# Kernel optimization log

Measured on AMD Instinct MI355X. Metric: run time of the kernel, lower is better.

The kernel has to match this reference:

```python
import jax, jax.numpy as jnp
import numpy as np

E = 8          # n_experts
TOPK = 2       # n_activated_experts
ROUTE_SCALE = 1.0
W_SCALE = 0.05  # keep conv outputs in a sane range


def _conv2d_same(x, w):
    # x: (B, Cin, H, W), w: (Cout, Cin, kh, kw) -> (B, Cout, H, W)
    return jax.lax.conv_general_dilated(
        x, w, window_strides=(1, 1), padding='SAME',
        dimension_numbers=('NCHW', 'OIHW', 'NCHW'))


def setup_inputs() -> dict:
    key = jax.random.key(0)
    ks = jax.random.split(key, 6)
    B, Cin, Cout, H, W = 4, 128, 128, 96, 96
    x = jax.random.normal(ks[0], (B, Cin, H, W), dtype=jnp.float32)
    gate_w = jax.random.normal(ks[1], (E, Cin, 3, 3), dtype=jnp.float32) * W_SCALE
    gate_bias = jnp.zeros((E,), dtype=jnp.float32)  # load-balance bias buffer (zeros in eval)
    expert_w = jax.random.normal(ks[2], (E, Cout, Cin, 3, 3), dtype=jnp.float32) * W_SCALE
    expert_b = jax.random.normal(ks[3], (E, Cout), dtype=jnp.float32) * W_SCALE
    shared_w = jax.random.normal(ks[4], (Cout, Cin, 3, 3), dtype=jnp.float32) * W_SCALE
    shared_b = jax.random.normal(ks[5], (Cout,), dtype=jnp.float32) * W_SCALE
    return {'x': x, 'gate_w': gate_w, 'gate_bias': gate_bias,
            'expert_w': expert_w, 'expert_b': expert_b,
            'shared_w': shared_w, 'shared_b': shared_b}


def reference(x, gate_w, gate_bias, expert_w, expert_b, shared_w, shared_b):
    B, Cin, H, W = x.shape
    Cout = shared_w.shape[0]

    # ---- Gate: sigmoid(conv) + bias buffer, per-pixel top-k over expert dim ----
    scores = jax.nn.sigmoid(_conv2d_same(x, gate_w))          # (B, E, H, W)
    biased = scores + gate_bias[None, :, None, None]
    scores_l = jnp.moveaxis(scores, 1, -1)                    # (B, H, W, E)
    biased_l = jnp.moveaxis(biased, 1, -1)
    _, idx = jax.lax.top_k(biased_l, TOPK)                    # (B, H, W, K)
    w_topk = jnp.take_along_axis(scores_l, idx, axis=-1)      # unbiased scores at topk
    w_topk = jax.nn.softmax(w_topk, axis=-1) * ROUTE_SCALE    # (B, H, W, K)

    # Per-pixel per-expert score: scatter topk weights back to E slots.
    onehot = jax.nn.one_hot(idx, E, dtype=x.dtype)            # (B, H, W, K, E)
    score_full = jnp.einsum('bhwke,bhwk->behw', onehot, w_topk)  # (B, E, H, W)

    # ---- Dense expert convs (all experts), then weighted accumulate ----
    ew = expert_w.reshape(E * Cout, Cin, 3, 3)
    eout = _conv2d_same(x, ew).reshape(B, E, Cout, H, W)
    eout = eout + expert_b[None, :, :, None, None]
    output = jnp.einsum('bechw,behw->bchw', eout, score_full)  # (B, Cout, H, W)

    # ---- Shared expert ----
    output = output + _conv2d_same(x, shared_w) + shared_b[None, :, None, None]
    return output
```

## Files before the change

### kernel.cpp

```cpp
#include <hip/hip_runtime.h>
#include <hip/hip_bf16.h>
#include <math.h>


typedef __attribute__((ext_vector_type(8))) short short8;
typedef __attribute__((ext_vector_type(4))) float f32x4;

static __device__ __forceinline__ unsigned short f2bf(float f) {
    unsigned int u = __float_as_uint(f);
    unsigned int r = (u + 0x7FFFu + ((u >> 16) & 1u)) >> 16;
    return (unsigned short)r;
}

__global__ __launch_bounds__(256) void gate_prep_kernel(
    const float* __restrict__ x, const float* __restrict__ gw,
    const float* __restrict__ gb,
    const float* __restrict__ ew, const float* __restrict__ sw,
    float* __restrict__ scores, unsigned short* __restrict__ pw)
{
    __shared__ alignas(16) char smem[45056];
    const int t  = threadIdx.x;
    const int bx = blockIdx.x;

    if (bx >= 576) {
        unsigned short* lt2 = reinterpret_cast<unsigned short*>(smem);
        const int pblk = bx - 576;
        const int e  = pblk >> 4;
        const int wv = (pblk >> 2) & 3;
        const int kc = pblk & 3;
        const float* src = (e < 8) ? (ew + e * 147456) : sw;
        const float* sb2 = src + (wv * 32) * 1152 + kc * 288;

        #pragma unroll
        for (int j = 0; j < 36; ++j) {
            int i = t + j * 256;
            int co_l = i / 288;
            int r    = i - co_l * 288;
            int k_l  = r / 9;
            int tap  = r - k_l * 9;
            float v = sb2[co_l * 1152 + r];
            lt2[tap * 1024 + (co_l >> 4) * 512 +
                ((k_l >> 3) * 16 + (co_l & 15)) * 8 + (k_l & 7)] = f2bf(v);
        }
        __syncthreads();

        uint4* pw16 = reinterpret_cast<uint4*>(pw);
        for (int c = t; c < 1152; c += 256) {
            int tap = c >> 7;
            int rem = c & 127;
            uint4 val = *reinterpret_cast<const uint4*>(&lt2[tap * 1024 + rem * 8]);
            pw16[(e * 9 + tap) * 2048 + wv * 512 + kc * 128 + rem] = val;
        }
        return;
    }

    float* gws = reinterpret_cast<float*>(smem);
    float (*red)[64][8] = reinterpret_cast<float (*)[64][8]>(smem + 36864);

    for (int i = t; i < 9216; i += 256) {
        int ci  = i / 72;
        int r   = i - ci * 72;
        int tap = r >> 3;
        int e   = r & 7;
        gws[i] = gw[(e * 128 + ci) * 9 + tap];
    }
    __syncthreads();

    const int g  = t >> 6;
    const int p  = t & 63;
    const int wt = bx % 3;
    const int h2 = (bx / 3) % 48;
    const int b  = bx / 144;
    const int h  = h2 * 2 + (p >> 5);
    const int w  = wt * 32 + (p & 31);

    int off[9]; float msk[9];
    #pragma unroll
    for (int kh = 0; kh < 3; kh++) {
        #pragma unroll
        for (int kw = 0; kw < 3; kw++) {
            int hh = h + kh - 1, ww = w + kw - 1;
            bool valid = (hh >= 0 && hh < 96 && ww >= 0 && ww < 96);
            int hc = min(max(hh, 0), 95), wc = min(max(ww, 0), 95);
            off[kh * 3 + kw] = hc * 96 + wc;
            msk[kh * 3 + kw] = valid ? 1.0f : 0.0f;
        }
    }

    const float* xb = x + (b * 128 + g * 32) * 9216;
    float acc[8] = {0.f,0.f,0.f,0.f,0.f,0.f,0.f,0.f};
    #pragma unroll 2
    for (int ci = 0; ci < 32; ci++) {
        const float* xc = xb + ci * 9216;
        const f32x4* wr4 = reinterpret_cast<const f32x4*>(&gws[(g * 32 + ci) * 72]);
        float xv[9];
        #pragma unroll
        for (int tap = 0; tap < 9; tap++) xv[tap] = xc[off[tap]] * msk[tap];
        #pragma unroll
        for (int tap = 0; tap < 9; tap++) {
            const f32x4 wa = wr4[tap * 2];
            const f32x4 wb = wr4[tap * 2 + 1];
            #pragma unroll
            for (int e0 = 0; e0 < 4; e0++) {
                acc[e0]     += xv[tap] * wa[e0];
                acc[e0 + 4] += xv[tap] * wb[e0];
            }
        }
    }

    #pragma unroll
    for (int e = 0; e < 8; e++) red[g][p][e] = acc[e];
    __syncthreads();

    if (t < 64) {
        float s[8], bs[8];
        #pragma unroll
        for (int e = 0; e < 8; e++) {
            float v = red[0][t][e] + red[1][t][e] + red[2][t][e] + red[3][t][e];
            s[e]  = 1.0f / (1.0f + expf(-v));
            bs[e] = s[e] + gb[e];
        }
        int i1 = 0; float b1 = bs[0]; float w1 = s[0];
        #pragma unroll
        for (int e = 1; e < 8; e++)
            if (bs[e] > b1) { b1 = bs[e]; i1 = e; w1 = s[e]; }
        int i2 = -1; float b2 = -1e30f; float w2 = 0.f;
        #pragma unroll
        for (int e = 0; e < 8; e++)
            if (e != i1 && bs[e] > b2) { b2 = bs[e]; i2 = e; w2 = s[e]; }

        float mx = fmaxf(w1, w2);
        float e1 = expf(w1 - mx), e2 = expf(w2 - mx);
        float inv = 1.0f / (e1 + e2);
        float p1 = e1 * inv, p2 = e2 * inv;

        const int hh = h2 * 2 + (t >> 5);
        const int ww = wt * 32 + (t & 31);
        int base = b * 8 * 9216 + hh * 96 + ww;
        #pragma unroll
        for (int e = 0; e < 8; e++) {
            float v = (e == i1) ? p1 : ((e == i2) ? p2 : 0.0f);
            scores[base + e * 9216] = v;
        }
    }
}

__global__ __launch_bounds__(256, 3) void moe_main_kernel(
    const float* __restrict__ x, const unsigned short* __restrict__ pw,
    const float* __restrict__ scores, const float* __restrict__ eb,
    const float* __restrict__ sb, float* __restrict__ out)
{
    __shared__ unsigned short xs[4 * 34 * 136];
    __shared__ float sc[8][64];
    __shared__ float bia[9][128];

    const int t  = threadIdx.x;
    const int bx = blockIdx.x;
    const int wt = bx % 3;
    const int h2 = (bx / 3) % 48;
    const int b  = bx / 144;
    const int h0 = h2 * 2, w0 = wt * 32;

    const float* xb = x + b * 128 * 9216;
    for (int i = t; i < 17408; i += 256) {
        int ci  = i / 136;
        int rem = i - ci * 136;
        int row = rem / 34;
        int col = rem - row * 34;
        int hh = h0 - 1 + row;
        int ww = w0 - 1 + col;
        float v = 0.0f;
        if (hh >= 0 && hh < 96 && ww >= 0 && ww < 96)
            v = xb[ci * 9216 + hh * 96 + ww];
        xs[(row * 34 + col) * 136 + ci] = f2bf(v);
    }
    for (int i = t; i < 512; i += 256) {
        int e = i >> 6, p = i & 63;
        sc[e][p] = scores[(b * 8 + e) * 9216 + (h0 + (p >> 5)) * 96 + (w0 + (p & 31))];
    }
    for (int i = t; i < 1152; i += 256) {
        int e = i >> 7, co = i & 127;
        bia[e][co] = (e < 8) ? eb[(e << 7) + co] : sb[co];
    }
    __syncthreads();

    const int wv = t >> 6;
    const int l  = t & 63;
    const int lm = l & 15;
    const int lq = l >> 4;

    f32x4 acc[2][4], accE[2][4];
    #pragma unroll
    for (int i2 = 0; i2 < 2; i2++)
        #pragma unroll
        for (int j = 0; j < 4; j++) {
            acc[i2][j]  = (f32x4){0.f, 0.f, 0.f, 0.f};
            accE[i2][j] = (f32x4){0.f, 0.f, 0.f, 0.f};
        }

    const int bBase = lm * 136 + lq * 8;
    const uint4* pw4 = reinterpret_cast<const uint4*>(pw) + wv * 512 + l;

    uint4 afA[8], afB[8];

#define LOADF(dst, etv) {                                                     \
    const uint4* _p = pw4 + (etv) * 2048;                                     \
    _Pragma("unroll")                                                         \
    for (int q = 0; q < 8; ++q) dst[q] = _p[(q >> 1) * 128 + (q & 1) * 64];   \
}

#define COMPUTE(src, etv) {                                                   \
    const int e_   = (etv) / 9;                                               \
    const int tap_ = (etv) - e_ * 9;                                          \
    const int kh_  = tap_ / 3;                                                \
    const int kw_  = tap_ - kh_ * 3;                                          \
    const int xr0  = kh_ * 4624 + kw_ * 136 + bBase;                          \
    _Pragma("unroll")                                                         \
    for (int kc = 0; kc < 4; ++kc) {                                          \
        const short8 a0 = *reinterpret_cast<const short8*>(&src[kc * 2 + 0]); \
        const short8 a1 = *reinterpret_cast<const short8*>(&src[kc * 2 + 1]); \
        _Pragma("unroll")                                                     \
        for (int j = 0; j < 4; ++j) {                                         \
            const short8 bv = *reinterpret_cast<const short8*>(               \
                &xs[xr0 + (j >> 1) * 4624 + (j & 1) * 2176 + kc * 32]);       \
            accE[0][j] = __builtin_amdgcn_mfma_f32_16x16x32_bf16(             \
                a0, bv, accE[0][j], 0, 0, 0);                                 \
            accE[1][j] = __builtin_amdgcn_mfma_f32_16x16x32_bf16(             \
                a1, bv, accE[1][j], 0, 0, 0);                                 \
        }                                                                     \
    }                                                                         \
    if (tap_ == 8) {                  \
        _Pragma("unroll")                                                     \
        for (int j = 0; j < 4; ++j) {                                         \
            const int p = j * 16 + lm;                                        \
            const float s_ = (e_ < 8) ? sc[e_][p] : 1.0f;                     \
            _Pragma("unroll")                                                 \
            for (int i2 = 0; i2 < 2; ++i2)                                    \
                _Pragma("unroll")                                             \
                for (int rr = 0; rr < 4; ++rr) {                              \
                    const int co_ = wv * 32 + i2 * 16 + lq * 4 + rr;          \
                    acc[i2][j][rr] += s_ * (accE[i2][j][rr] + bia[e_][co_]);  \
                    accE[i2][j][rr] = 0.f;                                    \
                }                                                             \
        }                                                                     \
    }                                                                         \
}

    LOADF(afA, 0);
    for (int eu = 0; eu < 40; ++eu) {
        const int et0 = eu * 2;
        LOADF(afB, et0 + 1);
        COMPUTE(afA, et0);
        LOADF(afA, et0 + 2);
        COMPUTE(afB, et0 + 1);
    }
    COMPUTE(afA, 80);
#undef COMPUTE
#undef LOADF

    float* ob = out + b * 128 * 9216;
    #pragma unroll
    for (int i2 = 0; i2 < 2; i2++)
        #pragma unroll
        for (int rr = 0; rr < 4; rr++) {
            const int co = wv * 32 + i2 * 16 + lq * 4 + rr;
            #pragma unroll
            for (int j = 0; j < 4; j++) {
                const int hh = h0 + (j >> 1);
                const int ww = w0 + (j & 1) * 16 + lm;
                ob[co * 9216 + hh * 96 + ww] = acc[i2][j][rr];
            }
        }
}

extern "C" void kernel_launch(void* const* d_in, const int* in_sizes, int n_in,
                              void* d_out, int out_size, void* d_ws, size_t ws_size,
                              hipStream_t stream) {
    const float* x  = (const float*)d_in[0];
    const float* gw = (const float*)d_in[1];
    const float* gb = (const float*)d_in[2];
    const float* ew = (const float*)d_in[3];
    const float* eb = (const float*)d_in[4];
    const float* sw = (const float*)d_in[5];
    const float* sb = (const float*)d_in[6];
    float* out = (float*)d_out;

    unsigned short* pw = (unsigned short*)d_ws;
    float* scores = (float*)((char*)d_ws + 2654208);

    gate_prep_kernel<<<720, 256, 0, stream>>>(x, gw, gb, ew, sw, scores, pw);
    moe_main_kernel<<<576, 256, 0, stream>>>(x, pw, scores, eb, sb, out);
}
```

Baseline: 221.1 us.

## Pad LDS pixel stride to 132 and keep gate weights in registers via readlane

The main kernel's x tile in shared memory now uses a per-pixel stride of 132 instead of 136 bf16, and the B operand is read as two 8-byte halves. The intent is to cut LDS bank conflicts on the MFMA operand reads. In the gate kernel, the staging of gate weights through shared memory is removed. Each lane now holds 36 weights in registers that are broadcast with readlane inside a fully unrolled channel loop, which avoids the LDS fill, its barrier and repeated LDS reads. The cost is higher register pressure and many scalar readlane instructions, and the 8-byte-aligned loads may issue more LDS instructions.

New measurement: 234.2 us. +5.9%, slower.

```diff
diff --git a/kernel.cpp b/kernel.cpp
--- a/kernel.cpp
+++ b/kernel.cpp
@@ -4,12 +4,23 @@
 
 
 typedef __attribute__((ext_vector_type(8))) short short8;
+typedef __attribute__((ext_vector_type(4))) short short4s;
 typedef __attribute__((ext_vector_type(4))) float f32x4;
 
 static __device__ __forceinline__ unsigned short f2bf(float f) {
     unsigned int u = __float_as_uint(f);
     unsigned int r = (u + 0x7FFFu + ((u >> 16) & 1u)) >> 16;
     return (unsigned short)r;
+}
+
+static __device__ __forceinline__ short8 ldsB(const unsigned short* p) {
+    short4s lo = *reinterpret_cast<const short4s*>(p);
+    short4s hi = *reinterpret_cast<const short4s*>(p + 4);
+    return __builtin_shufflevector(lo, hi, 0, 1, 2, 3, 4, 5, 6, 7);
+}
+
+static __device__ __forceinline__ float rdlane(float v, int lane) {
+    return __uint_as_float(__builtin_amdgcn_readlane(__float_as_uint(v), lane));
 }
 
 __global__ __launch_bounds__(256) void gate_prep_kernel(
@@ -18,12 +29,13 @@
     const float* __restrict__ ew, const float* __restrict__ sw,
     float* __restrict__ scores, unsigned short* __restrict__ pw)
 {
-    __shared__ alignas(16) char smem[45056];
+    __shared__ float red[4][64][8];
+    __shared__ unsigned short lt2[9216];
+
     const int t  = threadIdx.x;
     const int bx = blockIdx.x;
 
     if (bx >= 576) {
-        unsigned short* lt2 = reinterpret_cast<unsigned short*>(smem);
         const int pblk = bx - 576;
         const int e  = pblk >> 4;
         const int wv = (pblk >> 2) & 3;
@@ -54,18 +66,6 @@
         return;
     }
 
-    float* gws = reinterpret_cast<float*>(smem);
-    float (*red)[64][8] = reinterpret_cast<float (*)[64][8]>(smem + 36864);
-
-    for (int i = t; i < 9216; i += 256) {
-        int ci  = i / 72;
-        int r   = i - ci * 72;
-        int tap = r >> 3;
-        int e   = r & 7;
-        gws[i] = gw[(e * 128 + ci) * 9 + tap];
-    }
-    __syncthreads();
-
     const int g  = t >> 6;
     const int p  = t & 63;
     const int wt = bx % 3;
@@ -74,6 +74,19 @@
     const int h  = h2 * 2 + (p >> 5);
     const int w  = wt * 32 + (p & 31);
 
+    float wreg[36];
+    {
+        const int ci  = g * 32 + (p >> 1);
+        const int jb  = (p & 1) * 36;
+        #pragma unroll
+        for (int jj = 0; jj < 36; ++jj) {
+            int jglob = jb + jj;
+            int e   = jglob / 9;
+            int tap = jglob - e * 9;
+            wreg[jj] = gw[(e * 128 + ci) * 9 + tap];
+        }
+    }
+
     int off[9]; float msk[9];
     #pragma unroll
     for (int kh = 0; kh < 3; kh++) {
@@ -89,21 +102,20 @@
 
     const float* xb = x + (b * 128 + g * 32) * 9216;
     float acc[8] = {0.f,0.f,0.f,0.f,0.f,0.f,0.f,0.f};
-    #pragma unroll 2
+    #pragma unroll
     for (int ci = 0; ci < 32; ci++) {
         const float* xc = xb + ci * 9216;
-        const f32x4* wr4 = reinterpret_cast<const f32x4*>(&gws[(g * 32 + ci) * 72]);
         float xv[9];
         #pragma unroll
         for (int tap = 0; tap < 9; tap++) xv[tap] = xc[off[tap]] * msk[tap];
         #pragma unroll
-        for (int tap = 0; tap < 9; tap++) {
-            const f32x4 wa = wr4[tap * 2];
-            const f32x4 wb = wr4[tap * 2 + 1];
+        for (int e = 0; e < 8; e++) {
             #pragma unroll
-            for (int e0 = 0; e0 < 4; e0++) {
-                acc[e0]     += xv[tap] * wa[e0];
-                acc[e0 + 4] += xv[tap] * wb[e0];
+            for (int tap = 0; tap < 9; tap++) {
+                const int j = e * 9 + tap;
+                const float wv = (j < 36) ? rdlane(wreg[j], 2 * ci)
+                                          : rdlane(wreg[j - 36], 2 * ci + 1);
+                acc[e] += xv[tap] * wv;
             }
         }
     }
@@ -150,7 +162,7 @@
     const float* __restrict__ scores, const float* __restrict__ eb,
     const float* __restrict__ sb, float* __restrict__ out)
 {
-    __shared__ unsigned short xs[4 * 34 * 136];
+    __shared__ unsigned short xs[136 * 132];
     __shared__ float sc[8][64];
     __shared__ float bia[9][128];
 
@@ -164,15 +176,15 @@
     const float* xb = x + b * 128 * 9216;
     for (int i = t; i < 17408; i += 256) {
         int ci  = i / 136;
-        int rem = i - ci * 136;
-        int row = rem / 34;
-        int col = rem - row * 34;
+        int pix = i - ci * 136;
+        int row = pix / 34;
+        int col = pix - row * 34;
         int hh = h0 - 1 + row;
         int ww = w0 - 1 + col;
         float v = 0.0f;
         if (hh >= 0 && hh < 96 && ww >= 0 && ww < 96)
             v = xb[ci * 9216 + hh * 96 + ww];
-        xs[(row * 34 + col) * 136 + ci] = f2bf(v);
+        xs[pix * 132 + ci] = f2bf(v);
     }
     for (int i = t; i < 512; i += 256) {
         int e = i >> 6, p = i & 63;
@@ -198,7 +210,7 @@
             accE[i2][j] = (f32x4){0.f, 0.f, 0.f, 0.f};
         }
 
-    const int bBase = lm * 136 + lq * 8;
+    const int bBase = lm * 132 + lq * 8;
     const uint4* pw4 = reinterpret_cast<const uint4*>(pw) + wv * 512 + l;
 
     uint4 afA[8], afB[8];
@@ -214,15 +226,15 @@
     const int tap_ = (etv) - e_ * 9;                                          \
     const int kh_  = tap_ / 3;                                                \
     const int kw_  = tap_ - kh_ * 3;                                          \
-    const int xr0  = kh_ * 4624 + kw_ * 136 + bBase;                          \
+    const int xr0  = kh_ * 4488 + kw_ * 132 + bBase;                          \
     _Pragma("unroll")                                                         \
     for (int kc = 0; kc < 4; ++kc) {                                          \
         const short8 a0 = *reinterpret_cast<const short8*>(&src[kc * 2 + 0]); \
         const short8 a1 = *reinterpret_cast<const short8*>(&src[kc * 2 + 1]); \
         _Pragma("unroll")                                                     \
         for (int j = 0; j < 4; ++j) {                                         \
-            const short8 bv = *reinterpret_cast<const short8*>(               \
-                &xs[xr0 + (j >> 1) * 4624 + (j & 1) * 2176 + kc * 32]);       \
+            const short8 bv = ldsB(                                           \
+                &xs[xr0 + (j >> 1) * 4488 + (j & 1) * 2112 + kc * 32]);       \
             accE[0][j] = __builtin_amdgcn_mfma_f32_16x16x32_bf16(             \
                 a0, bv, accE[0][j], 0, 0, 0);                                 \
             accE[1][j] = __builtin_amdgcn_mfma_f32_16x16x32_bf16(             \
```

## Split Cin across wave pairs with larger per-wave M tile and LDS reduction

Applied to the files above, without the earlier changes.

Each wave now covers 64 output channels over half of the input channels (split-K across two wave pairs) instead of 32 channels over all 128. This doubles reuse of each LDS B fragment across four MFMA rows. A shared-memory reduction combines the two halves before the store. The LDS row pitch changes from 136 to 132 to alter bank mapping, B loads are split into two 8-byte reads, s_setprio is placed around the MFMA block, and occupancy drops to 2 blocks per SM to make room for the doubled accumulators.

Result: slower. 262.8 us (+18.9%).

```diff
diff --git a/kernel.cpp b/kernel.cpp
--- a/kernel.cpp
+++ b/kernel.cpp
@@ -4,12 +4,19 @@
 
 
 typedef __attribute__((ext_vector_type(8))) short short8;
+typedef __attribute__((ext_vector_type(4))) short short4s;
 typedef __attribute__((ext_vector_type(4))) float f32x4;
 
 static __device__ __forceinline__ unsigned short f2bf(float f) {
     unsigned int u = __float_as_uint(f);
     unsigned int r = (u + 0x7FFFu + ((u >> 16) & 1u)) >> 16;
     return (unsigned short)r;
+}
+
+static __device__ __forceinline__ short8 ldsB(const unsigned short* p) {
+    short4s lo = *reinterpret_cast<const short4s*>(p);
+    short4s hi = *reinterpret_cast<const short4s*>(p + 4);
+    return __builtin_shufflevector(lo, hi, 0, 1, 2, 3, 4, 5, 6, 7);
 }
 
 __global__ __launch_bounds__(256) void gate_prep_kernel(
@@ -145,12 +152,15 @@
     }
 }
 
-__global__ __launch_bounds__(256, 3) void moe_main_kernel(
+__global__ __launch_bounds__(256, 2) void moe_main_kernel(
     const float* __restrict__ x, const unsigned short* __restrict__ pw,
     const float* __restrict__ scores, const float* __restrict__ eb,
     const float* __restrict__ sb, float* __restrict__ out)
 {
-    __shared__ unsigned short xs[4 * 34 * 136];
+    __shared__ union {
+        unsigned short xs[136 * 132];
+        float red[8192];
+    } u;
     __shared__ float sc[8][64];
     __shared__ float bia[9][128];
 
@@ -164,15 +174,15 @@
     const float* xb = x + b * 128 * 9216;
     for (int i = t; i < 17408; i += 256) {
         int ci  = i / 136;
-        int rem = i - ci * 136;
-        int row = rem / 34;
-        int col = rem - row * 34;
+        int pix = i - ci * 136;
+        int row = pix / 34;
+        int col = pix - row * 34;
         int hh = h0 - 1 + row;
         int ww = w0 - 1 + col;
         float v = 0.0f;
         if (hh >= 0 && hh < 96 && ww >= 0 && ww < 96)
             v = xb[ci * 9216 + hh * 96 + ww];
-        xs[(row * 34 + col) * 136 + ci] = f2bf(v);
+        u.xs[pix * 132 + ci] = f2bf(v);
     }
     for (int i = t; i < 512; i += 256) {
         int e = i >> 6, p = i & 63;
@@ -184,29 +194,32 @@
     }
     __syncthreads();
 
-    const int wv = t >> 6;
-    const int l  = t & 63;
-    const int lm = l & 15;
-    const int lq = l >> 4;
-
-    f32x4 acc[2][4], accE[2][4];
+    const int wv4 = t >> 6;
+    const int cf  = wv4 & 1;
+    const int ch  = wv4 >> 1;
+    const int l   = t & 63;
+    const int lm  = l & 15;
+    const int lq  = l >> 4;
+
+    f32x4 acc[4][4], accE[4][4];
     #pragma unroll
-    for (int i2 = 0; i2 < 2; i2++)
+    for (int m = 0; m < 4; m++)
         #pragma unroll
         for (int j = 0; j < 4; j++) {
-            acc[i2][j]  = (f32x4){0.f, 0.f, 0.f, 0.f};
-            accE[i2][j] = (f32x4){0.f, 0.f, 0.f, 0.f};
-        }
-
-    const int bBase = lm * 136 + lq * 8;
-    const uint4* pw4 = reinterpret_cast<const uint4*>(pw) + wv * 512 + l;
+            acc[m][j]  = (f32x4){0.f, 0.f, 0.f, 0.f};
+            accE[m][j] = (f32x4){0.f, 0.f, 0.f, 0.f};
+        }
+
+    const int bBase = lm * 132 + ch * 64 + lq * 8;
+    const uint4* pw4 = reinterpret_cast<const uint4*>(pw) + cf * 1024 + ch * 256 + l;
 
     uint4 afA[8], afB[8];
 
 #define LOADF(dst, etv) {                                                     \
     const uint4* _p = pw4 + (etv) * 2048;                                     \
     _Pragma("unroll")                                                         \
-    for (int q = 0; q < 8; ++q) dst[q] = _p[(q >> 1) * 128 + (q & 1) * 64];   \
+    for (int q = 0; q < 8; ++q)                                               \
+        dst[q] = _p[(q >> 2) * 512 + ((q >> 1) & 1) * 128 + (q & 1) * 64];    \
 }
 
 #define COMPUTE(src, etv) {                                                   \
@@ -214,33 +227,38 @@
     const int tap_ = (etv) - e_ * 9;                                          \
     const int kh_  = tap_ / 3;                                                \
     const int kw_  = tap_ - kh_ * 3;                                          \
-    const int xr0  = kh_ * 4624 + kw_ * 136 + bBase;                          \
+    const int xr0  = kh_ * 4488 + kw_ * 132 + bBase;                          \
+    __builtin_amdgcn_s_setprio(1);                                            \
     _Pragma("unroll")                                                         \
-    for (int kc = 0; kc < 4; ++kc) {                                          \
-        const short8 a0 = *reinterpret_cast<const short8*>(&src[kc * 2 + 0]); \
-        const short8 a1 = *reinterpret_cast<const short8*>(&src[kc * 2 + 1]); \
+    for (int kc2 = 0; kc2 < 2; ++kc2) {                                       \
         _Pragma("unroll")                                                     \
         for (int j = 0; j < 4; ++j) {                                         \
-            const short8 bv = *reinterpret_cast<const short8*>(               \
-                &xs[xr0 + (j >> 1) * 4624 + (j & 1) * 2176 + kc * 32]);       \
-            accE[0][j] = __builtin_amdgcn_mfma_f32_16x16x32_bf16(             \
-                a0, bv, accE[0][j], 0, 0, 0);                                 \
-            accE[1][j] = __builtin_amdgcn_mfma_f32_16x16x32_bf16(             \
-                a1, bv, accE[1][j], 0, 0, 0);                                 \
+            const short8 bv = ldsB(                                           \
+                &u.xs[xr0 + (j >> 1) * 4488 + (j & 1) * 2112 + kc2 * 32]);    \
+            _Pragma("unroll")                                                 \
+            for (int a = 0; a < 2; ++a) {                                     \
+                accE[a*2+0][j] = __builtin_amdgcn_mfma_f32_16x16x32_bf16(     \
+                    *reinterpret_cast<const short8*>(&src[a*4 + kc2*2 + 0]),  \
+                    bv, accE[a*2+0][j], 0, 0, 0);                             \
+                accE[a*2+1][j] = __builtin_amdgcn_mfma_f32_16x16x32_bf16(     \
+                    *reinterpret_cast<const short8*>(&src[a*4 + kc2*2 + 1]),  \
+                    bv, accE[a*2+1][j], 0, 0, 0);                             \
+            }                                                                 \
         }                                                                     \
     }                                                                         \
-    if (tap_ == 8) {                  \
+    __builtin_amdgcn_s_setprio(0);                                            \
+    if (tap_ == 8) {      \
         _Pragma("unroll")                                                     \
         for (int j = 0; j < 4; ++j) {                                         \
-            const int p = j * 16 + lm;                                        \
-            const float s_ = (e_ < 8) ? sc[e_][p] : 1.0f;                     \
+            const float s_ = (e_ < 8) ? sc[e_][j * 16 + lm] : 1.0f;           \
             _Pragma("unroll")                                                 \
-            for (int i2 = 0; i2 < 2; ++i2)                                    \
+            for (int m = 0; m < 4; ++m)                                       \
                 _Pragma("unroll")                                             \
                 for (int rr = 0; rr < 4; ++rr) {                              \
-                    const int co_ = wv * 32 + i2 * 16 + lq * 4 + rr;          \
-                    acc[i2][j][rr] += s_ * (accE[i2][j][rr] + bia[e_][co_]);  \
-                    accE[i2][j][rr] = 0.f;                                    \
+                    const int co_ = cf*64 + (m>>1)*32 + (m&1)*16 + lq*4 + rr; \
+                    const float bb = (ch == 0) ? bia[e_][co_] : 0.0f;         \
+                    acc[m][j][rr] += s_ * (accE[m][j][rr] + bb);              \
+                    accE[m][j][rr] = 0.f;                                     \
                 }                                                             \
         }                                                                     \
     }                                                                         \
@@ -258,19 +276,34 @@
 #undef COMPUTE
 #undef LOADF
 
-    float* ob = out + b * 128 * 9216;
-    #pragma unroll
-    for (int i2 = 0; i2 < 2; i2++)
-        #pragma unroll
-        for (int rr = 0; rr < 4; rr++) {
-            const int co = wv * 32 + i2 * 16 + lq * 4 + rr;
+    __syncthreads();
+    if (ch == 1) {
+        #pragma unroll
+        for (int m = 0; m < 4; m++)
             #pragma unroll
-            for (int j = 0; j < 4; j++) {
-                const int hh = h0 + (j >> 1);
-                const int ww = w0 + (j & 1) * 16 + lm;
-                ob[co * 9216 + hh * 96 + ww] = acc[i2][j][rr];
+            for (int j = 0; j < 4; j++)
+                #pragma unroll
+                for (int rr = 0; rr < 4; rr++)
+                    u.red[((((cf * 4 + m) * 4 + j) * 4 + rr) << 6) + l] = acc[m][j][rr];
+    }
+    __syncthreads();
+    if (ch == 0) {
+        float* ob = out + b * 128 * 9216;
+        #pragma unroll
+        for (int m = 0; m < 4; m++)
+            #pragma unroll
+            for (int rr = 0; rr < 4; rr++) {
+                const int co = cf * 64 + (m >> 1) * 32 + (m & 1) * 16 + lq * 4 + rr;
+                #pragma unroll
+                for (int j = 0; j < 4; j++) {
+                    const float v = acc[m][j][rr] +
+                        u.red[((((cf * 4 + m) * 4 + j) * 4 + rr) << 6) + l];
+                    const int hh = h0 + (j >> 1);
+                    const int ww = w0 + (j & 1) * 16 + lm;
+                    ob[co * 9216 + hh * 96 + ww] = v;
+                }
             }
-        }
+    }
 }
 
 extern "C" void kernel_launch(void* const* d_in, const int* in_sizes, int n_in,
```
